# Performance work log

Hardware: AMD Instinct MI355X
Metric: run time of the kernel (lower is better)

Reference implementation:

```python
import jax, jax.numpy as jnp
import numpy as np

BETA = 1.0
GAMMA = 1.0
TAU = 1.0
EPS = 1e-8
RANK_CLAMP = 10  # torch.clamp(rank, max=10)


def _pearson(a, b):
    # a, b: [N, D]; pearson correlation along axis 1
    a = a - a.mean(axis=1, keepdims=True)
    b = b - b.mean(axis=1, keepdims=True)
    num = (a * b).sum(axis=1)
    den = jnp.linalg.norm(a, axis=1) * jnp.linalg.norm(b, axis=1) + EPS
    return num / den


def _filtered_ranks(y):
    # Vectorized equivalent of the per-row python loop: for each row, drop the
    # rank entry at the argmax position, yielding [B, C-1].
    B, C = y.shape
    j = jnp.argmax(y, axis=1)                       # [B]
    rank = jnp.minimum(jnp.argsort(y, axis=1), RANK_CLAMP)  # [B, C]
    base = jnp.arange(C - 1)[None, :]               # [1, C-1]
    idx = base + (base >= j[:, None]).astype(base.dtype)    # skip column j
    filt = jnp.take_along_axis(rank, idx, axis=1).astype(jnp.float32)
    return filt, j


def reference(z_s, z_t):
    y_s = jax.nn.softmax(z_s / TAU, axis=1)
    y_t = jax.nn.softmax(z_t / TAU, axis=1)

    # inter-class relation (spearman variant)
    fs, js = _filtered_ranks(y_s)
    ft, jt = _filtered_ranks(y_t)
    spearman = _pearson(fs, ft).mean()
    equal = (js == jt).astype(jnp.float32).mean()
    inter_loss = TAU ** 2 * (1.0 - (equal + spearman))

    # intra-class relation: pearson across batch per class
    intra_loss = TAU ** 2 * (1.0 - _pearson(y_s.T, y_t.T).mean())

    return BETA * inter_loss + GAMMA * intra_loss


def setup_inputs() -> dict:
    key = jax.random.key(0)
    k1, k2 = jax.random.split(key)
    B, C = 4096, 16000
    z_s = jax.random.normal(k1, (B, C), dtype=jnp.float32)
    z_t = jax.random.normal(k2, (B, C), dtype=jnp.float32)
    return {"z_s": z_s, "z_t": z_t}
```

## Files before the change

### kernel.cpp

```cpp
#include <hip/hip_runtime.h>
#include <math.h>

#define B_ROWS 4096
#define C_COLS 16000
#define NTH 10
static_assert((B_ROWS & (B_ROWS - 1)) == 0, "B pow2");

__device__ __forceinline__ void block_sum2(float& a, float& b) {
#pragma unroll
  for (int off = 32; off > 0; off >>= 1) {
    a += __shfl_down(a, off);
    b += __shfl_down(b, off);
  }
  __shared__ float sa[4], sb[4];
  const int w = threadIdx.x >> 6;
  if ((threadIdx.x & 63) == 0) { sa[w] = a; sb[w] = b; }
  __syncthreads();
  if (threadIdx.x == 0) {
    a = sa[0] + sa[1] + sa[2] + sa[3];
    b = sb[0] + sb[1] + sb[2] + sb[3];
  }
}

__global__ __launch_bounds__(256) void k_rowpass(
    const float* __restrict__ zs, const float* __restrict__ zt,
    float* __restrict__ rinv, int* __restrict__ jmax, int* __restrict__ pos)
{
  const int bid = blockIdx.x;
  const int m = bid >> 12;
  const int r = bid & (B_ROWS - 1);
  const float* __restrict__ z = (m ? zt : zs) + (size_t)r * C_COLS;

  float th[NTH];
#pragma unroll
  for (int i = 0; i < NTH; ++i) th[i] = z[i];

  int cnt[NTH];
#pragma unroll
  for (int i = 0; i < NTH; ++i) cnt[i] = 0;

  float vmax = -__builtin_inff();
  int vidx = 0;
  float sume = 0.f;

  const float4* __restrict__ z4 = (const float4*)z;
  for (int it = threadIdx.x; it < C_COLS / 4; it += 256) {
    const float4 v = z4[it];
    const int c = it * 4;
    const float xs[4] = {v.x, v.y, v.z, v.w};
#pragma unroll
    for (int u = 0; u < 4; ++u) {
      const float x = xs[u];
#pragma unroll
      for (int i = 0; i < NTH; ++i) cnt[i] += (x < th[i]) ? 1 : 0;
      if (x > vmax) { vmax = x; vidx = c + u; }
      sume += __expf(x);
    }
  }

#pragma unroll
  for (int off = 32; off > 0; off >>= 1) {
    sume += __shfl_down(sume, off);
#pragma unroll
    for (int i = 0; i < NTH; ++i) cnt[i] += __shfl_down(cnt[i], off);
    const float ov = __shfl_down(vmax, off);
    const int oi = __shfl_down(vidx, off);
    if (ov > vmax || (ov == vmax && oi < vidx)) { vmax = ov; vidx = oi; }
  }
  __shared__ float s_sum[4], s_max[4];
  __shared__ int s_idx[4], s_cnt[4][NTH];
  const int wave = threadIdx.x >> 6;
  if ((threadIdx.x & 63) == 0) {
    s_sum[wave] = sume; s_max[wave] = vmax; s_idx[wave] = vidx;
#pragma unroll
    for (int i = 0; i < NTH; ++i) s_cnt[wave][i] = cnt[i];
  }
  __syncthreads();
  if (threadIdx.x == 0) {
    float ts = 0.f, tm = s_max[0];
    int ti = s_idx[0];
    int tc[NTH];
#pragma unroll
    for (int i = 0; i < NTH; ++i) tc[i] = 0;
    for (int w = 0; w < 4; ++w) {
      ts += s_sum[w];
      if (s_max[w] > tm || (s_max[w] == tm && s_idx[w] < ti)) { tm = s_max[w]; ti = s_idx[w]; }
#pragma unroll
      for (int i = 0; i < NTH; ++i) tc[i] += s_cnt[w][i];
    }
    const int base = m * B_ROWS + r;
    rinv[base] = 1.f / ts;
    jmax[base] = ti;
#pragma unroll
    for (int i = 0; i < NTH; ++i) {
      int p = tc[i];
      for (int k = 0; k < i; ++k) p += (th[k] == th[i]) ? 1 : 0;
      pos[base * NTH + i] = p;
    }
  }
}

__global__ __launch_bounds__(256) void k_inter(
    const int* __restrict__ jmax, const int* __restrict__ pos,
    float* __restrict__ acc)
{
  const int r = blockIdx.x * 256 + threadIdx.x;
  float pear = 0.f, eq = 0.f;
  if (r < B_ROWS) {
    const int js = jmax[r];
    const int jt = jmax[B_ROWS + r];
    eq = (js == jt) ? 1.f : 0.f;
    int qs[NTH], qt[NTH];
    float vs[NTH], vt[NTH];
    int ns = 0, nt = 0;
    float sds = 0.f, sds2 = 0.f, sdt = 0.f, sdt2 = 0.f;
#pragma unroll
    for (int i = 0; i < NTH; ++i) {
      const float v = (float)(i - NTH);
      const int p = pos[r * NTH + i];
      if (p != js) {
        qs[ns] = p - (p > js ? 1 : 0);
        vs[ns] = v; ++ns;
        sds += v; sds2 += v * v;
      }
      const int p2 = pos[(B_ROWS + r) * NTH + i];
      if (p2 != jt) {
        qt[nt] = p2 - (p2 > jt ? 1 : 0);
        vt[nt] = v; ++nt;
        sdt += v; sdt2 += v * v;
      }
    }
    float sprod = 0.f;
    for (int a = 0; a < ns; ++a)
      for (int b = 0; b < nt; ++b)
        if (qs[a] == qt[b]) sprod += vs[a] * vt[b];
    const float Cm1 = (float)(C_COLS - 1);
    const float num  = sprod - sds * sdt / Cm1;
    const float vars = sds2 - sds * sds / Cm1;
    const float vart = sdt2 - sdt * sdt / Cm1;
    pear = num / (sqrtf(fmaxf(vars, 0.f)) * sqrtf(fmaxf(vart, 0.f)) + 1e-8f);
  }
  block_sum2(pear, eq);
  if (threadIdx.x == 0) {
    atomicAdd(&acc[0], pear);
    atomicAdd(&acc[1], eq);
  }
}

__global__ __launch_bounds__(256) void k_colpass(
    const float* __restrict__ zs, const float* __restrict__ zt,
    const float* __restrict__ rinv, float* __restrict__ colacc)
{
  const int c = blockIdx.x * 256 + threadIdx.x;
  const int r0 = blockIdx.y * 64;
  if (c >= C_COLS) return;
  float s1 = 0.f, s2 = 0.f, t1 = 0.f, t2 = 0.f, st = 0.f;
  size_t off = (size_t)r0 * C_COLS + (size_t)c;
#pragma unroll 4
  for (int k = 0; k < 64; ++k) {
    const float a = __expf(zs[off]) * rinv[r0 + k];
    const float b = __expf(zt[off]) * rinv[B_ROWS + r0 + k];
    s1 += a; s2 += a * a;
    t1 += b; t2 += b * b;
    st += a * b;
    off += C_COLS;
  }
  atomicAdd(&colacc[0 * C_COLS + c], s1);
  atomicAdd(&colacc[1 * C_COLS + c], t1);
  atomicAdd(&colacc[2 * C_COLS + c], s2);
  atomicAdd(&colacc[3 * C_COLS + c], t2);
  atomicAdd(&colacc[4 * C_COLS + c], st);
}

__global__ __launch_bounds__(256) void k_intra(
    const float* __restrict__ colacc, float* __restrict__ acc)
{
  const int c = blockIdx.x * 256 + threadIdx.x;
  float pear = 0.f, dummy = 0.f;
  if (c < C_COLS) {
    const float s1 = colacc[0 * C_COLS + c];
    const float t1 = colacc[1 * C_COLS + c];
    const float s2 = colacc[2 * C_COLS + c];
    const float t2 = colacc[3 * C_COLS + c];
    const float st = colacc[4 * C_COLS + c];
    const float Bf = (float)B_ROWS;
    const float num = st - s1 * t1 / Bf;
    const float vs = fmaxf(s2 - s1 * s1 / Bf, 0.f);
    const float vt = fmaxf(t2 - t1 * t1 / Bf, 0.f);
    pear = num / (sqrtf(vs) * sqrtf(vt) + 1e-8f);
  }
  block_sum2(pear, dummy);
  if (threadIdx.x == 0) atomicAdd(&acc[2], pear);
}

__global__ void k_final(const float* __restrict__ acc, float* __restrict__ out)
{
  if (threadIdx.x == 0) {
    const float spearman = acc[0] / (float)B_ROWS;
    const float eq = acc[1] / (float)B_ROWS;
    const float inter = 1.f - (eq + spearman);
    const float intra = 1.f - acc[2] / (float)C_COLS;
    out[0] = inter + intra;
  }
}

extern "C" void kernel_launch(void* const* d_in, const int* in_sizes, int n_in,
                              void* d_out, int out_size, void* d_ws, size_t ws_size,
                              hipStream_t stream) {
  const float* zs = (const float*)d_in[0];
  const float* zt = (const float*)d_in[1];
  float* out = (float*)d_out;
  float* ws = (float*)d_ws;

  float* rinv   = ws;
  int*   jmax   = (int*)(ws + 8192);
  int*   pos    = (int*)(ws + 16384);
  float* colacc = ws + 16384 + 81920;
  float* acc    = colacc + 5 * C_COLS;

  hipMemsetAsync(colacc, 0, (5 * C_COLS + 4) * sizeof(float), stream);

  k_rowpass<<<2 * B_ROWS, 256, 0, stream>>>(zs, zt, rinv, jmax, pos);
  k_inter<<<B_ROWS / 256, 256, 0, stream>>>(jmax, pos, acc);
  dim3 g3((C_COLS + 255) / 256, B_ROWS / 64);
  k_colpass<<<g3, 256, 0, stream>>>(zs, zt, rinv, colacc);
  k_intra<<<(C_COLS + 255) / 256, 256, 0, stream>>>(colacc, acc);
  k_final<<<1, 64, 0, stream>>>(acc, out);
}
```

Before: 619.7 us.

## Use ballot-popcount rank counting and float4 column pass loads

The row pass replaces per-lane threshold counters with wave-wide ballot plus popcount, which drops the per-counter shuffle reduction, and splits the exp sum into four independent accumulators. The column pass loads float4 vectors so each thread handles four adjacent columns, giving wider loads and a quarter as many threads along columns, at the cost of more registers and four times the atomics per thread. Launch order of the column and inter kernels is swapped. The ballot counts are now wave-uniform sums, so the later shared-memory sum across waves stays correct.

```diff
diff --git a/kernel.cpp b/kernel.cpp
--- a/kernel.cpp
+++ b/kernel.cpp
@@ -3,8 +3,10 @@
 
 #define B_ROWS 4096
 #define C_COLS 16000
+#define NQ 4000
 #define NTH 10
 static_assert((B_ROWS & (B_ROWS - 1)) == 0, "B pow2");
+static_assert(C_COLS % 4 == 0, "C mult of 4");
 
 __device__ __forceinline__ void block_sum2(float& a, float& b) {
 #pragma unroll
@@ -41,28 +43,46 @@
 
   float vmax = -__builtin_inff();
   int vidx = 0;
-  float sume = 0.f;
+  float se0 = 0.f, se1 = 0.f, se2 = 0.f, se3 = 0.f;
 
   const float4* __restrict__ z4 = (const float4*)z;
-  for (int it = threadIdx.x; it < C_COLS / 4; it += 256) {
+  for (int it = threadIdx.x; it < NQ; it += 256) {
     const float4 v = z4[it];
     const int c = it * 4;
-    const float xs[4] = {v.x, v.y, v.z, v.w};
-#pragma unroll
-    for (int u = 0; u < 4; ++u) {
-      const float x = xs[u];
-#pragma unroll
-      for (int i = 0; i < NTH; ++i) cnt[i] += (x < th[i]) ? 1 : 0;
-      if (x > vmax) { vmax = x; vidx = c + u; }
-      sume += __expf(x);
-    }
-  }
+    {
+      const float x = v.x;
+#pragma unroll
+      for (int i = 0; i < NTH; ++i) cnt[i] += (int)__popcll(__ballot(x < th[i]));
+      if (x > vmax) { vmax = x; vidx = c; }
+      se0 += __expf(x);
+    }
+    {
+      const float x = v.y;
+#pragma unroll
+      for (int i = 0; i < NTH; ++i) cnt[i] += (int)__popcll(__ballot(x < th[i]));
+      if (x > vmax) { vmax = x; vidx = c + 1; }
+      se1 += __expf(x);
+    }
+    {
+      const float x = v.z;
+#pragma unroll
+      for (int i = 0; i < NTH; ++i) cnt[i] += (int)__popcll(__ballot(x < th[i]));
+      if (x > vmax) { vmax = x; vidx = c + 2; }
+      se2 += __expf(x);
+    }
+    {
+      const float x = v.w;
+#pragma unroll
+      for (int i = 0; i < NTH; ++i) cnt[i] += (int)__popcll(__ballot(x < th[i]));
+      if (x > vmax) { vmax = x; vidx = c + 3; }
+      se3 += __expf(x);
+    }
+  }
+  float sume = (se0 + se1) + (se2 + se3);
 
 #pragma unroll
   for (int off = 32; off > 0; off >>= 1) {
     sume += __shfl_down(sume, off);
-#pragma unroll
-    for (int i = 0; i < NTH; ++i) cnt[i] += __shfl_down(cnt[i], off);
     const float ov = __shfl_down(vmax, off);
     const int oi = __shfl_down(vidx, off);
     if (ov > vmax || (ov == vmax && oi < vidx)) { vmax = ov; vidx = oi; }
@@ -147,29 +167,57 @@
   }
 }
 
+#define RPB 64
 __global__ __launch_bounds__(256) void k_colpass(
     const float* __restrict__ zs, const float* __restrict__ zt,
     const float* __restrict__ rinv, float* __restrict__ colacc)
 {
-  const int c = blockIdx.x * 256 + threadIdx.x;
-  const int r0 = blockIdx.y * 64;
-  if (c >= C_COLS) return;
-  float s1 = 0.f, s2 = 0.f, t1 = 0.f, t2 = 0.f, st = 0.f;
-  size_t off = (size_t)r0 * C_COLS + (size_t)c;
+  const int q = blockIdx.x * 256 + threadIdx.x;
+  const int r0 = blockIdx.y * RPB;
+  if (q >= NQ) return;
+  const float4* __restrict__ zs4 = (const float4*)zs;
+  const float4* __restrict__ zt4 = (const float4*)zt;
+
+  float4 s1 = {0,0,0,0}, s2 = {0,0,0,0}, t1 = {0,0,0,0}, t2 = {0,0,0,0}, st = {0,0,0,0};
+  size_t off = (size_t)r0 * NQ + (size_t)q;
 #pragma unroll 4
-  for (int k = 0; k < 64; ++k) {
-    const float a = __expf(zs[off]) * rinv[r0 + k];
-    const float b = __expf(zt[off]) * rinv[B_ROWS + r0 + k];
-    s1 += a; s2 += a * a;
-    t1 += b; t2 += b * b;
-    st += a * b;
-    off += C_COLS;
-  }
-  atomicAdd(&colacc[0 * C_COLS + c], s1);
-  atomicAdd(&colacc[1 * C_COLS + c], t1);
-  atomicAdd(&colacc[2 * C_COLS + c], s2);
-  atomicAdd(&colacc[3 * C_COLS + c], t2);
-  atomicAdd(&colacc[4 * C_COLS + c], st);
+  for (int k = 0; k < RPB; ++k) {
+    const float ra = rinv[r0 + k];
+    const float rb = rinv[B_ROWS + r0 + k];
+    const float4 va = zs4[off];
+    const float4 vb = zt4[off];
+    float a, b;
+    a = __expf(va.x) * ra; b = __expf(vb.x) * rb;
+    s1.x += a; s2.x += a * a; t1.x += b; t2.x += b * b; st.x += a * b;
+    a = __expf(va.y) * ra; b = __expf(vb.y) * rb;
+    s1.y += a; s2.y += a * a; t1.y += b; t2.y += b * b; st.y += a * b;
+    a = __expf(va.z) * ra; b = __expf(vb.z) * rb;
+    s1.z += a; s2.z += a * a; t1.z += b; t2.z += b * b; st.z += a * b;
+    a = __expf(va.w) * ra; b = __expf(vb.w) * rb;
+    s1.w += a; s2.w += a * a; t1.w += b; t2.w += b * b; st.w += a * b;
+    off += NQ;
+  }
+  const int c = q * 4;
+  atomicAdd(&colacc[0 * C_COLS + c + 0], s1.x);
+  atomicAdd(&colacc[0 * C_COLS + c + 1], s1.y);
+  atomicAdd(&colacc[0 * C_COLS + c + 2], s1.z);
+  atomicAdd(&colacc[0 * C_COLS + c + 3], s1.w);
+  atomicAdd(&colacc[1 * C_COLS + c + 0], t1.x);
+  atomicAdd(&colacc[1 * C_COLS + c + 1], t1.y);
+  atomicAdd(&colacc[1 * C_COLS + c + 2], t1.z);
+  atomicAdd(&colacc[1 * C_COLS + c + 3], t1.w);
+  atomicAdd(&colacc[2 * C_COLS + c + 0], s2.x);
+  atomicAdd(&colacc[2 * C_COLS + c + 1], s2.y);
+  atomicAdd(&colacc[2 * C_COLS + c + 2], s2.z);
+  atomicAdd(&colacc[2 * C_COLS + c + 3], s2.w);
+  atomicAdd(&colacc[3 * C_COLS + c + 0], t2.x);
+  atomicAdd(&colacc[3 * C_COLS + c + 1], t2.y);
+  atomicAdd(&colacc[3 * C_COLS + c + 2], t2.z);
+  atomicAdd(&colacc[3 * C_COLS + c + 3], t2.w);
+  atomicAdd(&colacc[4 * C_COLS + c + 0], st.x);
+  atomicAdd(&colacc[4 * C_COLS + c + 1], st.y);
+  atomicAdd(&colacc[4 * C_COLS + c + 2], st.z);
+  atomicAdd(&colacc[4 * C_COLS + c + 3], st.w);
 }
 
 __global__ __launch_bounds__(256) void k_intra(
@@ -221,9 +269,9 @@
   hipMemsetAsync(colacc, 0, (5 * C_COLS + 4) * sizeof(float), stream);
 
   k_rowpass<<<2 * B_ROWS, 256, 0, stream>>>(zs, zt, rinv, jmax, pos);
+  dim3 g3((NQ + 255) / 256, B_ROWS / RPB);
+  k_colpass<<<g3, 256, 0, stream>>>(zs, zt, rinv, colacc);
   k_inter<<<B_ROWS / 256, 256, 0, stream>>>(jmax, pos, acc);
-  dim3 g3((C_COLS + 255) / 256, B_ROWS / 64);
-  k_colpass<<<g3, 256, 0, stream>>>(zs, zt, rinv, colacc);
   k_intra<<<(C_COLS + 255) / 256, 256, 0, stream>>>(colacc, acc);
   k_final<<<1, 64, 0, stream>>>(acc, out);
 }
```

Measured after the change: 671.7 us. +8.4%, slower.
